# Performance work log

Hardware: AMD Instinct MI355X
Metric: run time of the kernel (lower is better)

## Reference

```python
import jax, jax.numpy as jnp
import numpy as np

WINDOW = (6, 7, 7)  # (agent_size, window_size, window_size)
HEADS = 8           # dim // dim_head = 256 // 32


def _relative_position_index(ws):
    d, h, w = ws
    coords = np.stack(np.meshgrid(np.arange(d), np.arange(h), np.arange(w), indexing='ij'))
    cf = coords.reshape(3, -1)                      # [3, n]
    rel = cf[:, :, None] - cf[:, None, :]           # [3, n, n]
    rel = rel.transpose(1, 2, 0).copy()             # [n, n, 3]
    rel[..., 0] += d - 1
    rel[..., 1] += h - 1
    rel[..., 2] += w - 1
    rel[..., 0] *= (2 * h - 1) * (2 * w - 1)
    rel[..., 1] *= (2 * w - 1)
    return rel.sum(-1)                              # [n, n] int

REL_IDX = jnp.asarray(_relative_position_index(WINDOW))


def setup_inputs() -> dict:
    key = jax.random.key(0)
    ks = jax.random.split(key, 7)
    dim = 256
    n_bias = (2 * WINDOW[0] - 1) * (2 * WINDOW[1] - 1) * (2 * WINDOW[2] - 1)  # 1859
    s = 0.02
    return {
        'x': jax.random.normal(ks[0], (2, 6, 12, 12, 7, 7, dim), jnp.float32),
        'Wq': jax.random.normal(ks[1], (dim, dim), jnp.float32) * s,
        'bq': jax.random.normal(ks[2], (dim,), jnp.float32) * s,
        'Wkv': jax.random.normal(ks[3], (dim, 2 * dim), jnp.float32) * s,
        'bkv': jax.random.normal(ks[4], (2 * dim,), jnp.float32) * s,
        'Wout': jax.random.normal(ks[5], (dim, dim), jnp.float32) * s,
        'bias_table': jax.random.normal(ks[6], (n_bias, HEADS), jnp.float32) * s,
    }


def reference(x, Wq, bq, Wkv, bkv, Wout, bias_table):
    b, l, gx, gy, w1, w2, d = x.shape
    h = HEADS
    dh = d // h
    n = l * w1 * w2
    B = b * gx * gy
    # 'b l x y w1 w2 d -> (b x y) (l w1 w2) d'  (agent-major token order)
    xt = jnp.transpose(x, (0, 2, 3, 1, 4, 5, 6)).reshape(B, n, d)
    q = xt @ Wq + bq                                  # [B, n, d]
    kv = xt @ Wkv + bkv                               # [B, n, 2d]
    k, v = kv[..., :d], kv[..., d:]
    split = lambda t: t.reshape(B, n, h, dh).transpose(0, 2, 1, 3)  # [B, h, n, dh]
    q, k, v = split(q), split(k), split(v)
    scale = dh ** -0.5
    sim = jnp.einsum('bhid,bhjd->bhij', q * scale, k)  # [B, h, n, n]
    bias = bias_table[REL_IDX]                         # [n, n, h]
    sim = sim + jnp.transpose(bias, (2, 0, 1))[None]
    attn = jax.nn.softmax(sim, axis=-1)
    out = jnp.einsum('bhij,bhjd->bhid', attn, v)       # [B, h, n, dh]
    out = out.transpose(0, 2, 1, 3).reshape(B, n, d) @ Wout
    # '(b x y) (l w1 w2) d -> b l x y w1 w2 d'
    out = out.reshape(b, gx, gy, l, w1, w2, d)
    return jnp.transpose(out, (0, 3, 1, 2, 4, 5, 6))
```

## Files before the change

### kernel.cpp

```cpp
#include <hip/hip_runtime.h>
#include <hip/hip_bf16.h>

#define DIM    256
#define NWIN   294
#define BWIN   288
#define MROWS  (BWIN * NWIN)
#define MPAD   84736
#define NHEADS 8
#define DH     32
#define NBIAS  1859

typedef __attribute__((ext_vector_type(8))) short  short8;
typedef __attribute__((ext_vector_type(4))) float  f32x4;

__device__ __forceinline__ unsigned short f2bf(float f) {
    unsigned int u = __float_as_uint(f);
    u += 0x7FFFu + ((u >> 16) & 1u);
    return (unsigned short)(u >> 16);
}

__device__ __forceinline__ unsigned pk2bf(float a, float b) {
    __hip_bfloat162 h = __float22bfloat162_rn(float2{a, b});
    unsigned u;
    __builtin_memcpy(&u, &h, 4);
    return u;
}

__device__ __forceinline__ void gl_lds16(const void* g, void* l) {
    __builtin_amdgcn_global_load_lds((const __attribute__((address_space(1))) unsigned int*)g,
                                     (__attribute__((address_space(3))) unsigned int*)l,
                                     16, 0, 0);
}

__global__ __launch_bounds__(256) void prep_x(const float* __restrict__ x,
                                              unsigned short* __restrict__ Xb)
{
    const int g   = blockIdx.x * 256 + threadIdx.x;
    const int row = g >> 5;
    const int col = (g & 31) * 8;
    if (row >= MPAD) return;
    uint4 pk;
    if (row < MROWS) {
        const int bw = row / NWIN, rw = row - bw * NWIN;
        const int bb = bw / 144,  r2 = bw - bb * 144;
        const int gxi = r2 / 12,  gyi = r2 - gxi * 12;
        const int lz = rw / 49,   r3 = rw - lz * 49;
        const int wa = r3 / 7,    wb = r3 - wa * 7;
        const float* src = x + ((((((size_t)bb * 6 + lz) * 12 + gxi) * 12 + gyi) * 7 + wa) * 7 + wb) * DIM + col;
        const float4 f0 = *(const float4*)(src);
        const float4 f1 = *(const float4*)(src + 4);
        pk.x = pk2bf(f0.x, f0.y);
        pk.y = pk2bf(f0.z, f0.w);
        pk.z = pk2bf(f1.x, f1.y);
        pk.w = pk2bf(f1.z, f1.w);
    } else {
        pk = (uint4){0u, 0u, 0u, 0u};
    }
    *(uint4*)(Xb + (size_t)row * 256 + col) = pk;
}

__global__ __launch_bounds__(256) void prep_w(const float* __restrict__ Wq,
                                              const float* __restrict__ Wkv,
                                              const float* __restrict__ Wout,
                                              unsigned short* __restrict__ Wt,
                                              unsigned short* __restrict__ Wot)
{
    const int g = blockIdx.x * 256 + threadIdx.x;
    if (g < 768 * 256) {
        const int n = g >> 8, k = g & 255;
        const float v = (n < 256) ? Wq[k * 256 + n] : Wkv[k * 512 + (n - 256)];
        Wt[g] = f2bf(v);
    } else {
        const int g2 = g - 768 * 256;
        const int n = g2 >> 8, k = g2 & 255;
        Wot[g2] = f2bf(Wout[k * 256 + n]);
    }
}

__global__ __launch_bounds__(256) void gemm_qkv(
    const unsigned short* __restrict__ Xb, const unsigned short* __restrict__ Wt,
    const float* __restrict__ bq, const float* __restrict__ bkv,
    unsigned short* __restrict__ Qb, unsigned short* __restrict__ Kb,
    unsigned short* __restrict__ Vtb)
{
    __shared__ __align__(16) unsigned short As[128 * 64];
    __shared__ __align__(16) unsigned short Bs[128 * 64];

    const int bn = blockIdx.x % 6;
    const int bm = blockIdx.x / 6;
    const int tileM = bm * 128;
    const int tileN = bn * 128;

    const int t    = threadIdx.x;
    const int w    = t >> 6;
    const int lane = t & 63;
    const int quad = lane >> 4;
    const int l15  = lane & 15;
    const int wm   = w >> 1, wn = w & 1;

    const int rA = lane >> 3;
    const int kA = (lane & 7) * 8;
    const unsigned short* aBase = Xb + ((size_t)tileM + rA) * 256 + kA;
    const unsigned short* bBase = Wt + ((size_t)tileN + rA) * 256 + kA;

    f32x4 acc[4][4] = {};

    for (int kb = 0; kb < 4; ++kb) {
        const int k0 = kb * 64;
        __syncthreads();
#pragma unroll
        for (int i = 0; i < 4; ++i) {
            const int c = w * 4 + i;
            gl_lds16(aBase + (size_t)c * 8 * 256 + k0, &As[c * 512]);
            gl_lds16(bBase + (size_t)c * 8 * 256 + k0, &Bs[c * 512]);
        }
        __syncthreads();
#pragma unroll
        for (int c2 = 0; c2 < 2; ++c2) {
            const int kk = c2 * 32 + quad * 8;
            short8 a[4], b[4];
#pragma unroll
            for (int mi = 0; mi < 4; ++mi)
                a[mi] = *(const short8*)&As[(wm * 64 + mi * 16 + l15) * 64 + kk];
#pragma unroll
            for (int ni = 0; ni < 4; ++ni)
                b[ni] = *(const short8*)&Bs[(wn * 64 + ni * 16 + l15) * 64 + kk];
#pragma unroll
            for (int mi = 0; mi < 4; ++mi)
#pragma unroll
                for (int ni = 0; ni < 4; ++ni)
                    acc[mi][ni] = __builtin_amdgcn_mfma_f32_16x16x32_bf16(a[mi], b[ni], acc[mi][ni], 0, 0, 0);
        }
    }

    const int colB = tileN + wn * 64;
    float bias[4];
#pragma unroll
    for (int ni = 0; ni < 4; ++ni) {
        const int n = colB + ni * 16 + l15;
        bias[ni] = (n < 256) ? bq[n] : bkv[n - 256];
    }
    const int rowB = tileM + wm * 64 + quad * 4;
#pragma unroll
    for (int mi = 0; mi < 4; ++mi) {
#pragma unroll
        for (int r = 0; r < 4; ++r) {
            const int row = rowB + mi * 16 + r;
            if (row < MROWS) {
                const int bw = row / NWIN;
                const int rw = row - bw * NWIN;
#pragma unroll
                for (int ni = 0; ni < 4; ++ni) {
                    const int n = colB + ni * 16 + l15;
                    const unsigned short v = f2bf(acc[mi][ni][r] + bias[ni]);
                    const int ch = n & 255;
                    const int hd = ch >> 5, di = ch & 31;
                    if (n < 512) {
                        unsigned short* dst = (n < 256) ? Qb : Kb;
                        dst[((size_t)(bw * NHEADS + hd) * NWIN + rw) * DH + di] = v;
                    } else {
                        Vtb[((size_t)(bw * NHEADS + hd) * DH + di) * NWIN + rw] = v;
                    }
                }
            }
        }
    }
}

__global__ __launch_bounds__(256, 3) void attn_kernel(
    const unsigned short* __restrict__ Qb, const unsigned short* __restrict__ Kb,
    const unsigned short* __restrict__ Vtb, const float* __restrict__ bias_table,
    unsigned short* __restrict__ Ob)
{
    const int bh   = blockIdx.x;
    const int bwin = bh >> 3;
    const int h    = bh & 7;

    __shared__ __align__(16) unsigned short Ks[304 * 40];
    __shared__ __align__(16) unsigned short Vts[32 * 328];
    __shared__ float          biasHs[NBIAS];
    __shared__ __align__(8) unsigned short cIdx[304];

    const int t    = threadIdx.x;
    const int w    = t >> 6;
    const int lane = t & 63;
    const int quad = lane >> 4;
    const int l15  = lane & 15;

    {
        const unsigned short* Kg = Kb + (size_t)bh * (NWIN * DH);
        for (int i = t; i < 304 * 4; i += 256) {
            const int row = i >> 2, seg = i & 3;
            uint4 v = (uint4){0u, 0u, 0u, 0u};
            if (row < NWIN) v = *(const uint4*)(Kg + row * 32 + seg * 8);
            *(uint4*)(Ks + row * 40 + seg * 8) = v;
        }
    }
    {
        const unsigned short* Vg = Vtb + (size_t)bh * (DH * NWIN);
        for (int i = t; i < 32 * 328; i += 256) {
            const int r = i / 328, c = i - r * 328;
            Vts[i] = (c < NWIN) ? Vg[r * NWIN + c] : (unsigned short)0;
        }
    }
    for (int i = t; i < NBIAS; i += 256) biasHs[i] = bias_table[i * NHEADS + h] * 1.44269504088896f;
    for (int i = t; i < 304; i += 256) {
        if (i < NWIN) {
            const int l = i / 49, r = i - l * 49;
            cIdx[i] = (unsigned short)(169 * l + 13 * (r / 7) + (r - (r / 7) * 7));
        } else cIdx[i] = 0;
    }
    __syncthreads();

    const float SL2E = 0.25503486f;
    const unsigned short* Qg = Qb + (size_t)bh * (NWIN * DH);
    const int   srcB = ((quad & 1) << 5) + l15;
    const bool  hiSel = (quad >= 2);
    const short8 ones = (short8){0x3F80,0x3F80,0x3F80,0x3F80,0x3F80,0x3F80,0x3F80,0x3F80};

#pragma unroll
    for (int r5 = 0; r5 < 5; ++r5) {
        const int it = 4 * r5 + w;
        if (it < 19) {
            short8 qf;
            const int qrow = it * 16 + l15;
            if (qrow < NWIN) qf = *(const short8*)(Qg + qrow * DH + quad * 8);
            else             qf = (short8){0,0,0,0,0,0,0,0};

            const int ciB = (int)cIdx[it * 16 + l15] + 929;
            const float* bbase = biasHs + ciB;

            f32x4 S[19];
#pragma unroll
            for (int jt = 0; jt < 19; ++jt) {
                const short8 kf = *(const short8*)(Ks + (jt * 16 + l15) * 40 + quad * 8);
                S[jt] = __builtin_amdgcn_mfma_f32_16x16x32_bf16(kf, qf, (f32x4){0.f,0.f,0.f,0.f}, 0, 0, 0);
            }

            unsigned pk0[20], pk1[20];
            pk0[19] = 0u; pk1[19] = 0u;
#pragma unroll
            for (int jt = 0; jt < 19; ++jt) {
                const ushort4 c4 = *(const ushort4*)(cIdx + jt * 16 + quad * 4);
                float p0 = exp2f(fmaf(S[jt][0], SL2E, bbase[-(int)c4.x]));
                float p1 = exp2f(fmaf(S[jt][1], SL2E, bbase[-(int)c4.y]));
                float p2 = exp2f(fmaf(S[jt][2], SL2E, bbase[-(int)c4.z]));
                float p3 = exp2f(fmaf(S[jt][3], SL2E, bbase[-(int)c4.w]));
                if (jt == 18) {
                    if (quad * 4 + 0 >= 6) p0 = 0.f;
                    if (quad * 4 + 1 >= 6) p1 = 0.f;
                    if (quad * 4 + 2 >= 6) p2 = 0.f;
                    if (quad * 4 + 3 >= 6) p3 = 0.f;
                }
                pk0[jt] = pk2bf(p0, p1);
                pk1[jt] = pk2bf(p2, p3);
            }

            f32x4 o0 = {0.f,0.f,0.f,0.f}, o1 = {0.f,0.f,0.f,0.f}, o2 = {0.f,0.f,0.f,0.f};
#pragma unroll
            for (int kt = 0; kt < 10; ++kt) {
                const int e0 = (int)pk0[2 * kt], e1 = (int)pk0[2 * kt + 1];
                const int f0 = (int)pk1[2 * kt], f1 = (int)pk1[2 * kt + 1];
                const unsigned aLo = (unsigned)__shfl(e0, srcB);
                const unsigned aHi = (unsigned)__shfl(e1, srcB);
                const unsigned bLo = (unsigned)__shfl(f0, srcB);
                const unsigned bHi = (unsigned)__shfl(f1, srcB);
                const unsigned cLo = (unsigned)__shfl(e0, srcB + 16);
                const unsigned cHi = (unsigned)__shfl(e1, srcB + 16);
                const unsigned dLo = (unsigned)__shfl(f0, srcB + 16);
                const unsigned dHi = (unsigned)__shfl(f1, srcB + 16);
                uint4 pw;
                pw.x = hiSel ? aHi : aLo;
                pw.y = hiSel ? bHi : bLo;
                pw.z = hiSel ? cHi : cLo;
                pw.w = hiSel ? dHi : dLo;
                short8 pa;
                __builtin_memcpy(&pa, &pw, 16);
                const short8 v0 = *(const short8*)(Vts + l15 * 328 + kt * 32 + quad * 8);
                const short8 v1 = *(const short8*)(Vts + (16 + l15) * 328 + kt * 32 + quad * 8);
                o0 = __builtin_amdgcn_mfma_f32_16x16x32_bf16(pa, v0, o0, 0, 0, 0);
                o1 = __builtin_amdgcn_mfma_f32_16x16x32_bf16(pa, v1, o1, 0, 0, 0);
                o2 = __builtin_amdgcn_mfma_f32_16x16x32_bf16(pa, ones, o2, 0, 0, 0);
            }

#pragma unroll
            for (int r = 0; r < 4; ++r) {
                const int rg = it * 16 + quad * 4 + r;
                if (rg < NWIN) {
                    const float inv = 1.0f / o2[r];
                    unsigned short* op = Ob + ((size_t)bwin * NWIN + rg) * DIM + h * DH;
                    op[l15]      = f2bf(o0[r] * inv);
                    op[16 + l15] = f2bf(o1[r] * inv);
                }
            }
        }
    }
}

__global__ __launch_bounds__(256) void gemm_out(
    const unsigned short* __restrict__ Ob, const unsigned short* __restrict__ Wot,
    float* __restrict__ out)
{
    __shared__ __align__(16) unsigned short As[128 * 64];
    __shared__ __align__(16) unsigned short Bs[128 * 64];

    const int bn = blockIdx.x & 1;
    const int bm = blockIdx.x >> 1;
    const int tileM = bm * 128;
    const int tileN = bn * 128;

    const int t    = threadIdx.x;
    const int w    = t >> 6;
    const int lane = t & 63;
    const int quad = lane >> 4;
    const int l15  = lane & 15;
    const int wm   = w >> 1, wn = w & 1;

    const int rA = lane >> 3;
    const int kA = (lane & 7) * 8;
    const unsigned short* aBase = Ob  + ((size_t)tileM + rA) * 256 + kA;
    const unsigned short* bBase = Wot + ((size_t)tileN + rA) * 256 + kA;

    f32x4 acc[4][4] = {};

    for (int kb = 0; kb < 4; ++kb) {
        const int k0 = kb * 64;
        __syncthreads();
#pragma unroll
        for (int i = 0; i < 4; ++i) {
            const int c = w * 4 + i;
            gl_lds16(aBase + (size_t)c * 8 * 256 + k0, &As[c * 512]);
            gl_lds16(bBase + (size_t)c * 8 * 256 + k0, &Bs[c * 512]);
        }
        __syncthreads();
#pragma unroll
        for (int c2 = 0; c2 < 2; ++c2) {
            const int kk = c2 * 32 + quad * 8;
            short8 a[4], b[4];
#pragma unroll
            for (int mi = 0; mi < 4; ++mi)
                a[mi] = *(const short8*)&As[(wm * 64 + mi * 16 + l15) * 64 + kk];
#pragma unroll
            for (int ni = 0; ni < 4; ++ni)
                b[ni] = *(const short8*)&Bs[(wn * 64 + ni * 16 + l15) * 64 + kk];
#pragma unroll
            for (int mi = 0; mi < 4; ++mi)
#pragma unroll
                for (int ni = 0; ni < 4; ++ni)
                    acc[mi][ni] = __builtin_amdgcn_mfma_f32_16x16x32_bf16(a[mi], b[ni], acc[mi][ni], 0, 0, 0);
        }
    }

    const int colB = tileN + wn * 64;
    const int rowB = tileM + wm * 64 + quad * 4;
#pragma unroll
    for (int mi = 0; mi < 4; ++mi) {
#pragma unroll
        for (int r = 0; r < 4; ++r) {
            const int row = rowB + mi * 16 + r;
            if (row < MROWS) {
                const int bw = row / NWIN, rw = row - bw * NWIN;
                const int bb = bw / 144,  r2 = bw - bb * 144;
                const int gxi = r2 / 12,  gyi = r2 - gxi * 12;
                const int lz = rw / 49,   r3 = rw - lz * 49;
                const int wa = r3 / 7,    wb = r3 - wa * 7;
                float* orow = out + ((((((size_t)bb * 6 + lz) * 12 + gxi) * 12 + gyi) * 7 + wa) * 7 + wb) * DIM;
#pragma unroll
                for (int ni = 0; ni < 4; ++ni)
                    orow[colB + ni * 16 + l15] = acc[mi][ni][r];
            }
        }
    }
}

extern "C" void kernel_launch(void* const* d_in, const int* in_sizes, int n_in,
                              void* d_out, int out_size, void* d_ws, size_t ws_size,
                              hipStream_t stream)
{
    const float* x          = (const float*)d_in[0];
    const float* Wq         = (const float*)d_in[1];
    const float* bq         = (const float*)d_in[2];
    const float* Wkv        = (const float*)d_in[3];
    const float* bkv        = (const float*)d_in[4];
    const float* Wout       = (const float*)d_in[5];
    const float* bias_table = (const float*)d_in[6];
    float* out = (float*)d_out;

    const size_t planePad = (size_t)MPAD * DIM;
    const size_t plane    = (size_t)MROWS * DIM;
    unsigned short* Xb  = (unsigned short*)d_ws;
    unsigned short* Qb  = Xb + planePad;
    unsigned short* Kb  = Qb + plane;
    unsigned short* Vtb = Kb + plane;
    unsigned short* Ob  = Vtb + plane;
    unsigned short* Wt  = Ob + planePad;
    unsigned short* Wot = Wt + 768 * 256;

    prep_x<<<MPAD / 8, 256, 0, stream>>>(x, Xb);
    prep_w<<<1024, 256, 0, stream>>>(Wq, Wkv, Wout, Wt, Wot);
    gemm_qkv<<<662 * 6, 256, 0, stream>>>(Xb, Wt, bq, bkv, Qb, Kb, Vtb);
    attn_kernel<<<BWIN * NHEADS, 256, 0, stream>>>(Qb, Kb, Vtb, bias_table, Ob);
    gemm_out<<<662 * 2, 256, 0, stream>>>(Ob, Wot, out);
}
```

Measured before the change: 439.8 us.

## Precompute dense bias matrix and permute V layout to drop P shuffles

Adds a prep kernel that expands the relative-position bias table into a dense per-head 304x304 matrix in global memory. The attention kernel then reads four contiguous bias values per MFMA tile instead of doing cIdx gathers from LDS. It also stores V^T in LDS with a permuted key order that matches the register layout of the exp'd scores, so the 8 cross-lane shuffles per k-step are no longer needed. The trade is an extra ~3 MB bias matrix read from global/L2 by every block, and a more complex V staging loop.

After: 406.0 us. 7.7% less time.

```diff
diff --git a/kernel.cpp b/kernel.cpp
--- a/kernel.cpp
+++ b/kernel.cpp
@@ -9,6 +9,7 @@
 #define NHEADS 8
 #define DH     32
 #define NBIAS  1859
+#define QPAD   304
 
 typedef __attribute__((ext_vector_type(8))) short  short8;
 typedef __attribute__((ext_vector_type(4))) float  f32x4;
@@ -77,6 +78,24 @@
     }
 }
 
+__global__ __launch_bounds__(256) void prep_bias(const float* __restrict__ bias_table,
+                                                 float* __restrict__ biasT)
+{
+    const int g = blockIdx.x * 256 + threadIdx.x;
+    if (g >= NHEADS * QPAD * QPAD) return;
+    const int k = g % QPAD;
+    const int q = (g / QPAD) % QPAD;
+    const int h = g / (QPAD * QPAD);
+    float v = 0.f;
+    if (q < NWIN && k < NWIN) {
+        const int ql = q / 49, qr = q - ql * 49, qa = qr / 7, qb = qr - qa * 7;
+        const int kl = k / 49, kr = k - kl * 49, ka = kr / 7, kb = kr - ka * 7;
+        const int idx = 169 * (ql - kl + 5) + 13 * (qa - ka + 6) + (qb - kb + 6);
+        v = bias_table[idx * NHEADS + h] * 1.44269504088896f;
+    }
+    biasT[g] = v;
+}
+
 __global__ __launch_bounds__(256) void gemm_qkv(
     const unsigned short* __restrict__ Xb, const unsigned short* __restrict__ Wt,
     const float* __restrict__ bq, const float* __restrict__ bkv,
@@ -169,7 +188,7 @@
 
 __global__ __launch_bounds__(256, 3) void attn_kernel(
     const unsigned short* __restrict__ Qb, const unsigned short* __restrict__ Kb,
-    const unsigned short* __restrict__ Vtb, const float* __restrict__ bias_table,
+    const unsigned short* __restrict__ Vtb, const float* __restrict__ biasT,
     unsigned short* __restrict__ Ob)
 {
     const int bh   = blockIdx.x;
@@ -178,8 +197,6 @@
 
     __shared__ __align__(16) unsigned short Ks[304 * 40];
     __shared__ __align__(16) unsigned short Vts[32 * 328];
-    __shared__ float          biasHs[NBIAS];
-    __shared__ __align__(8) unsigned short cIdx[304];
 
     const int t    = threadIdx.x;
     const int w    = t >> 6;
@@ -198,24 +215,30 @@
     }
     {
         const unsigned short* Vg = Vtb + (size_t)bh * (DH * NWIN);
-        for (int i = t; i < 32 * 328; i += 256) {
-            const int r = i / 328, c = i - r * 328;
-            Vts[i] = (c < NWIN) ? Vg[r * NWIN + c] : (unsigned short)0;
-        }
-    }
-    for (int i = t; i < NBIAS; i += 256) biasHs[i] = bias_table[i * NHEADS + h] * 1.44269504088896f;
-    for (int i = t; i < 304; i += 256) {
-        if (i < NWIN) {
-            const int l = i / 49, r = i - l * 49;
-            cIdx[i] = (unsigned short)(169 * l + 13 * (r / 7) + (r - (r / 7) * 7));
-        } else cIdx[i] = 0;
+        for (int i = t; i < 32 * 80; i += 256) {
+            const int d = i / 80, c = i - d * 80;
+            const int kt = c >> 3, qd = (c >> 1) & 3, hf = c & 1;
+            const int kb = kt * 32 + hf * 16 + qd * 4;
+            unsigned int u0 = 0u, u1 = 0u;
+            if (kb + 3 < NWIN) {
+                u0 = *(const unsigned int*)(Vg + d * NWIN + kb);
+                u1 = *(const unsigned int*)(Vg + d * NWIN + kb + 2);
+            } else if (kb < NWIN) {
+                unsigned short r0 = Vg[d * NWIN + kb];
+                unsigned short r1 = (kb + 1 < NWIN) ? Vg[d * NWIN + kb + 1] : (unsigned short)0;
+                unsigned short r2 = (kb + 2 < NWIN) ? Vg[d * NWIN + kb + 2] : (unsigned short)0;
+                u0 = (unsigned int)r0 | ((unsigned int)r1 << 16);
+                u1 = (unsigned int)r2;
+            }
+            unsigned int* dst = (unsigned int*)(Vts + d * 328 + c * 4);
+            dst[0] = u0; dst[1] = u1;
+        }
     }
     __syncthreads();
 
     const float SL2E = 0.25503486f;
     const unsigned short* Qg = Qb + (size_t)bh * (NWIN * DH);
-    const int   srcB = ((quad & 1) << 5) + l15;
-    const bool  hiSel = (quad >= 2);
+    const float* biasH = biasT + (size_t)h * QPAD * QPAD;
     const short8 ones = (short8){0x3F80,0x3F80,0x3F80,0x3F80,0x3F80,0x3F80,0x3F80,0x3F80};
 
 #pragma unroll
@@ -227,8 +250,7 @@
             if (qrow < NWIN) qf = *(const short8*)(Qg + qrow * DH + quad * 8);
             else             qf = (short8){0,0,0,0,0,0,0,0};
 
-            const int ciB = (int)cIdx[it * 16 + l15] + 929;
-            const float* bbase = biasHs + ciB;
+            const float* bb = biasH + (size_t)qrow * QPAD;
 
             f32x4 S[19];
 #pragma unroll
@@ -241,11 +263,11 @@
             pk0[19] = 0u; pk1[19] = 0u;
 #pragma unroll
             for (int jt = 0; jt < 19; ++jt) {
-                const ushort4 c4 = *(const ushort4*)(cIdx + jt * 16 + quad * 4);
-                float p0 = exp2f(fmaf(S[jt][0], SL2E, bbase[-(int)c4.x]));
-                float p1 = exp2f(fmaf(S[jt][1], SL2E, bbase[-(int)c4.y]));
-                float p2 = exp2f(fmaf(S[jt][2], SL2E, bbase[-(int)c4.z]));
-                float p3 = exp2f(fmaf(S[jt][3], SL2E, bbase[-(int)c4.w]));
+                const f32x4 b4 = *(const f32x4*)(bb + jt * 16 + quad * 4);
+                float p0 = exp2f(fmaf(S[jt][0], SL2E, b4[0]));
+                float p1 = exp2f(fmaf(S[jt][1], SL2E, b4[1]));
+                float p2 = exp2f(fmaf(S[jt][2], SL2E, b4[2]));
+                float p3 = exp2f(fmaf(S[jt][3], SL2E, b4[3]));
                 if (jt == 18) {
                     if (quad * 4 + 0 >= 6) p0 = 0.f;
                     if (quad * 4 + 1 >= 6) p1 = 0.f;
@@ -259,21 +281,11 @@
             f32x4 o0 = {0.f,0.f,0.f,0.f}, o1 = {0.f,0.f,0.f,0.f}, o2 = {0.f,0.f,0.f,0.f};
 #pragma unroll
             for (int kt = 0; kt < 10; ++kt) {
-                const int e0 = (int)pk0[2 * kt], e1 = (int)pk0[2 * kt + 1];
-                const int f0 = (int)pk1[2 * kt], f1 = (int)pk1[2 * kt + 1];
-                const unsigned aLo = (unsigned)__shfl(e0, srcB);
-                const unsigned aHi = (unsigned)__shfl(e1, srcB);
-                const unsigned bLo = (unsigned)__shfl(f0, srcB);
-                const unsigned bHi = (unsigned)__shfl(f1, srcB);
-                const unsigned cLo = (unsigned)__shfl(e0, srcB + 16);
-                const unsigned cHi = (unsigned)__shfl(e1, srcB + 16);
-                const unsigned dLo = (unsigned)__shfl(f0, srcB + 16);
-                const unsigned dHi = (unsigned)__shfl(f1, srcB + 16);
                 uint4 pw;
-                pw.x = hiSel ? aHi : aLo;
-                pw.y = hiSel ? bHi : bLo;
-                pw.z = hiSel ? cHi : cLo;
-                pw.w = hiSel ? dHi : dLo;
+                pw.x = pk0[2 * kt];
+                pw.y = pk1[2 * kt];
+                pw.z = pk0[2 * kt + 1];
+                pw.w = pk1[2 * kt + 1];
                 short8 pa;
                 __builtin_memcpy(&pa, &pw, 16);
                 const short8 v0 = *(const short8*)(Vts + l15 * 328 + kt * 32 + quad * 8);
@@ -395,10 +407,12 @@
     unsigned short* Ob  = Vtb + plane;
     unsigned short* Wt  = Ob + planePad;
     unsigned short* Wot = Wt + 768 * 256;
+    float*          biasT = (float*)(Wot + 256 * 256);
 
     prep_x<<<MPAD / 8, 256, 0, stream>>>(x, Xb);
     prep_w<<<1024, 256, 0, stream>>>(Wq, Wkv, Wout, Wt, Wot);
+    prep_bias<<<(NHEADS * QPAD * QPAD + 255) / 256, 256, 0, stream>>>(bias_table, biasT);
     gemm_qkv<<<662 * 6, 256, 0, stream>>>(Xb, Wt, bq, bkv, Qb, Kb, Vtb);
-    attn_kernel<<<BWIN * NHEADS, 256, 0, stream>>>(Qb, Kb, Vtb, bias_table, Ob);
+    attn_kernel<<<BWIN * NHEADS, 256, 0, stream>>>(Qb, Kb, Vtb, biasT, Ob);
     gemm_out<<<662 * 2, 256, 0, stream>>>(Ob, Wot, out);
 }
```
